# Kernel optimization log

Measured on AMD Instinct MI355X. Metric: run time of the kernel, lower is better.

## Reference

```python
import jax, jax.numpy as jnp
import numpy as np

B, H, S, D1, D2 = 1, 8, 4096, 64, 64


def setup_inputs() -> dict:
    key = jax.random.key(0)
    ks = jax.random.split(key, 6)
    q = jax.random.normal(ks[0], (B, H, S, D1), dtype=jnp.float32)
    k = jax.random.normal(ks[1], (B, H, S, D1), dtype=jnp.float32)
    v = jax.random.normal(ks[2], (B, H, S, D2), dtype=jnp.float32)
    # Decay coefficients per head/position (positive, like RetNet gamma^i masks)
    coef_q = jax.random.uniform(ks[3], (H, S), dtype=jnp.float32)
    coef_k = jax.random.uniform(ks[4], (H, S), dtype=jnp.float32)
    # Normalizer must be bounded away from 0
    mask_normer = jax.random.uniform(ks[5], (H, S), dtype=jnp.float32) + 0.5
    return {"q": q, "k": k, "v": v, "coef_q": coef_q, "coef_k": coef_k,
            "mask_normer": mask_normer}


def _rmsenorm(x):
    return x * jax.lax.rsqrt(jnp.mean(x * x, axis=-1, keepdims=True) + 1e-6)


def reference(q, k, v, coef_q, coef_k, mask_normer):
    # q,k: [B,H,S,D1]; v: [B,H,S,D2]; coef_*/mask_normer: [H,S]
    q_bar = q * (coef_q / mask_normer)[None, :, :, None]      # [B,H,S,D1]
    k_bar = k * coef_k[None, :, :, None]                       # [B,H,S,D1]
    # running normalization P_i = |q_i . sum_{j<=i} k_j|, clamped at 1
    T = jnp.cumsum(k_bar, axis=-2)                             # [B,H,S,D1]
    P = jnp.einsum('bhid,bhid->bhi', T, q_bar)                 # [B,H,S]
    P = jnp.maximum(jnp.abs(jax.lax.stop_gradient(P)), 1.0)[..., None]
    q_bar = q_bar / P
    # outer-product state and prefix sum over sequence
    D = jnp.einsum('bhia,bhic->bhiac', k_bar, v)               # [B,H,S,D1,D2]
    D = jnp.cumsum(D, axis=-3)                                 # cumsum over S
    O = jnp.einsum('bhia,bhiac->bhic', q_bar, D)               # [B,H,S,D2]
    return _rmsenorm(O)
```

## Files before the change

### kernel.cpp

```cpp
#include <hip/hip_runtime.h>

#define H 8
#define S 4096
#define D 64
#define C 64
#define NC (S / C)
#define PITCH 72

typedef short bf16x8 __attribute__((ext_vector_type(8)));
typedef float f32x4 __attribute__((ext_vector_type(4)));

struct alignas(16) F4 { float v[4]; };

__device__ inline short rne_bf16(float x) {
  unsigned u = __builtin_bit_cast(unsigned, x);
  unsigned r = u + 0x7fffu + ((u >> 16) & 1u);
  return (short)(r >> 16);
}
__device__ inline float bf16_to_f(short h) {
  unsigned u = ((unsigned)(unsigned short)h) << 16;
  return __builtin_bit_cast(float, u);
}

__global__ __launch_bounds__(256) void k_chunk_sums(
    const float* __restrict__ k, const float* __restrict__ v,
    const float* __restrict__ coef_k, float* __restrict__ wsKV) {
  const int ch = blockIdx.x, h = blockIdx.y, t = threadIdx.x;
  __shared__ float kb[C][D + 4];
  __shared__ float vb[C][D + 4];

  const float* kp = k + (size_t)(h * S + ch * C) * D;
  const float* vp = v + (size_t)(h * S + ch * C) * D;
  const float* ck = coef_k + h * S + ch * C;

#pragma unroll
  for (int r = 0; r < 4; ++r) {
    int o = 1024 * r + 4 * t;
    int i = o >> 6, d = o & 63;
    F4 kv = *reinterpret_cast<const F4*>(kp + o);
    F4 vv = *reinterpret_cast<const F4*>(vp + o);
    float c = ck[i];
#pragma unroll
    for (int u = 0; u < 4; ++u) kv.v[u] *= c;
    *reinterpret_cast<F4*>(&kb[i][d]) = kv;
    *reinterpret_cast<F4*>(&vb[i][d]) = vv;
  }
  __syncthreads();

  const int tc = t >> 4, ta = t & 15;
  float acc[4][4];
#pragma unroll
  for (int a = 0; a < 4; ++a)
#pragma unroll
    for (int b = 0; b < 4; ++b) acc[a][b] = 0.f;

  for (int i = 0; i < C; ++i) {
    F4 vc = *reinterpret_cast<const F4*>(&vb[i][4 * tc]);
    F4 ka = *reinterpret_cast<const F4*>(&kb[i][4 * ta]);
#pragma unroll
    for (int cc = 0; cc < 4; ++cc)
#pragma unroll
      for (int aa = 0; aa < 4; ++aa) acc[cc][aa] += vc.v[cc] * ka.v[aa];
  }
  float* dst = wsKV + (size_t)(h * NC + ch) * (D * D);
#pragma unroll
  for (int cc = 0; cc < 4; ++cc) {
    F4 w;
#pragma unroll
    for (int aa = 0; aa < 4; ++aa) w.v[aa] = acc[cc][aa];
    *reinterpret_cast<F4*>(dst + (4 * tc + cc) * D + 4 * ta) = w;
  }
}

__global__ __launch_bounds__(128) void k_scan(float* __restrict__ wsKV) {
  const int seg = blockIdx.x, h = blockIdx.y, t = threadIdx.x;
  const int e0 = seg * 128 + t;
  unsigned* wp = reinterpret_cast<unsigned*>(wsKV);
  float run = 0.f;
  for (int base = 0; base < NC; base += 8) {
    float x[8];
#pragma unroll
    for (int u = 0; u < 8; ++u)
      x[u] = wsKV[(size_t)(h * NC + base + u) * (D * D) + e0];
#pragma unroll
    for (int u = 0; u < 8; ++u) {
      short hi = rne_bf16(run);
      short lo = rne_bf16(run - bf16_to_f(hi));
      wp[(size_t)(h * NC + base + u) * (D * D) + e0] =
          (((unsigned)(unsigned short)lo) << 16) | (unsigned)(unsigned short)hi;
      run += x[u];
    }
  }
}

__global__ __launch_bounds__(256) void k_chunk_out(
    const float* __restrict__ q, const float* __restrict__ k,
    const float* __restrict__ v,
    const float* __restrict__ coef_q, const float* __restrict__ coef_k,
    const float* __restrict__ mask_normer,
    const float* __restrict__ wsKV, float* __restrict__ out) {
  const int ch = blockIdx.x, h = blockIdx.y, t = threadIdx.x;
  __shared__ alignas(16) short qb[C * PITCH];
  __shared__ alignas(16) short kbf[C * PITCH];
  __shared__ alignas(16) short s0h[D * PITCH];
  __shared__ alignas(16) short s0l[D * PITCH];
  __shared__ alignas(16) short vT[D * PITCH];
  __shared__ alignas(16) short Ab[C * PITCH];

  const size_t base = (size_t)(h * S + ch * C) * D;
  const float* qp = q + base;
  const float* kp = k + base;
  const float* cq = coef_q + h * S + ch * C;
  const float* ck = coef_k + h * S + ch * C;
  const float* mn = mask_normer + h * S + ch * C;
  const unsigned* s0p =
      reinterpret_cast<const unsigned*>(wsKV) + (size_t)(h * NC + ch) * (D * D);

  {
    const int i = t >> 2, c0 = (t & 3) * 16;
    const float sq = cq[i] / mn[i];
    const float sk = ck[i];
    bf16x8 wq[2], wk[2], wh[2], wl[2];
#pragma unroll
    for (int g = 0; g < 2; ++g) {
#pragma unroll
      for (int u0 = 0; u0 < 8; u0 += 4) {
        F4 qv = *reinterpret_cast<const F4*>(qp + i * D + c0 + 8 * g + u0);
        F4 kv = *reinterpret_cast<const F4*>(kp + i * D + c0 + 8 * g + u0);
#pragma unroll
        for (int u = 0; u < 4; ++u) {
          wq[g][u0 + u] = rne_bf16(qv.v[u] * sq);
          wk[g][u0 + u] = rne_bf16(kv.v[u] * sk);
        }
      }
#pragma unroll
      for (int u = 0; u < 8; ++u) {
        unsigned p = s0p[i * D + c0 + 8 * g + u];
        wh[g][u] = (short)(p & 0xffffu);
        wl[g][u] = (short)(p >> 16);
      }
    }
#pragma unroll
    for (int g = 0; g < 2; ++g) {
      *reinterpret_cast<bf16x8*>(&qb[i * PITCH + c0 + 8 * g]) = wq[g];
      *reinterpret_cast<bf16x8*>(&kbf[i * PITCH + c0 + 8 * g]) = wk[g];
      *reinterpret_cast<bf16x8*>(&s0h[i * PITCH + c0 + 8 * g]) = wh[g];
      *reinterpret_cast<bf16x8*>(&s0l[i * PITCH + c0 + 8 * g]) = wl[g];
    }
  }
  {
    const int c = t >> 2, i0 = (t & 3) * 16;
    const float* vcol = v + base + c;
    bf16x8 wv[2];
#pragma unroll
    for (int g = 0; g < 2; ++g)
#pragma unroll
      for (int u = 0; u < 8; ++u)
        wv[g][u] = rne_bf16(vcol[(size_t)(i0 + 8 * g + u) * D]);
    *reinterpret_cast<bf16x8*>(&vT[c * PITCH + i0]) = wv[0];
    *reinterpret_cast<bf16x8*>(&vT[c * PITCH + i0 + 8]) = wv[1];
  }
  __syncthreads();

  const int lane = t & 63, w = t >> 6;
  const int arow = lane & 15, kg = lane >> 4;
  const int rbase = (16 * w + arow) * PITCH + 8 * kg;

  bf16x8 qa0 = *reinterpret_cast<const bf16x8*>(&qb[rbase]);
  bf16x8 qa1 = *reinterpret_cast<const bf16x8*>(&qb[rbase + 32]);

  f32x4 accA[4];
#pragma unroll
  for (int n = 0; n < 4; ++n) {
    const int bb = (16 * n + arow) * PITCH + 8 * kg;
    bf16x8 b0 = *reinterpret_cast<const bf16x8*>(&kbf[bb]);
    bf16x8 b1 = *reinterpret_cast<const bf16x8*>(&kbf[bb + 32]);
    f32x4 z = {0.f, 0.f, 0.f, 0.f};
    z = __builtin_amdgcn_mfma_f32_16x16x32_bf16(qa0, b0, z, 0, 0, 0);
    z = __builtin_amdgcn_mfma_f32_16x16x32_bf16(qa1, b1, z, 0, 0, 0);
    accA[n] = z;
  }
#pragma unroll
  for (int n = 0; n < 4; ++n)
#pragma unroll
    for (int r = 0; r < 4; ++r) {
      int i = 4 * kg + r;
      int j = 16 * n + arow;
      float x = (j <= 16 * w + i) ? accA[n][r] : 0.f;
      Ab[(16 * w + i) * PITCH + j] = rne_bf16(x);
    }

  bf16x8 aa0 = *reinterpret_cast<const bf16x8*>(&Ab[rbase]);
  bf16x8 aa1 = *reinterpret_cast<const bf16x8*>(&Ab[rbase + 32]);
  f32x4 accO[4];
#pragma unroll
  for (int n = 0; n < 4; ++n) {
    const int bb = (16 * n + arow) * PITCH + 8 * kg;
    bf16x8 h0 = *reinterpret_cast<const bf16x8*>(&s0h[bb]);
    bf16x8 h1 = *reinterpret_cast<const bf16x8*>(&s0h[bb + 32]);
    bf16x8 l0 = *reinterpret_cast<const bf16x8*>(&s0l[bb]);
    bf16x8 l1 = *reinterpret_cast<const bf16x8*>(&s0l[bb + 32]);
    bf16x8 v0 = *reinterpret_cast<const bf16x8*>(&vT[bb]);
    bf16x8 v1 = *reinterpret_cast<const bf16x8*>(&vT[bb + 32]);
    f32x4 z = {0.f, 0.f, 0.f, 0.f};
    z = __builtin_amdgcn_mfma_f32_16x16x32_bf16(qa0, h0, z, 0, 0, 0);
    z = __builtin_amdgcn_mfma_f32_16x16x32_bf16(qa1, h1, z, 0, 0, 0);
    z = __builtin_amdgcn_mfma_f32_16x16x32_bf16(qa0, l0, z, 0, 0, 0);
    z = __builtin_amdgcn_mfma_f32_16x16x32_bf16(qa1, l1, z, 0, 0, 0);
    z = __builtin_amdgcn_mfma_f32_16x16x32_bf16(aa0, v0, z, 0, 0, 0);
    z = __builtin_amdgcn_mfma_f32_16x16x32_bf16(aa1, v1, z, 0, 0, 0);
    accO[n] = z;
  }

  float* op = out + base;
#pragma unroll
  for (int r = 0; r < 4; ++r) {
    const int i = 16 * w + 4 * kg + r;
    float ss = 0.f;
#pragma unroll
    for (int n = 0; n < 4; ++n) ss += accO[n][r] * accO[n][r];
#pragma unroll
    for (int off = 1; off < 16; off <<= 1) ss += __shfl_xor(ss, off);
    const float sc = rsqrtf(ss * (1.0f / D) + 1e-6f);
#pragma unroll
    for (int n = 0; n < 4; ++n)
      op[(size_t)i * D + 16 * n + arow] = accO[n][r] * sc;
  }
}

extern "C" void kernel_launch(void* const* d_in, const int* in_sizes, int n_in,
                              void* d_out, int out_size, void* d_ws, size_t ws_size,
                              hipStream_t stream) {
  (void)in_sizes; (void)n_in; (void)out_size; (void)ws_size;
  const float* q  = (const float*)d_in[0];
  const float* k  = (const float*)d_in[1];
  const float* v  = (const float*)d_in[2];
  const float* cq = (const float*)d_in[3];
  const float* ck = (const float*)d_in[4];
  const float* mn = (const float*)d_in[5];
  float* out = (float*)d_out;

  float* wsKV = (float*)d_ws;

  k_chunk_sums<<<dim3(NC, H), dim3(256), 0, stream>>>(k, v, ck, wsKV);
  k_scan<<<dim3(32, H), dim3(128), 0, stream>>>(wsKV);
  k_chunk_out<<<dim3(NC, H), dim3(256), 0, stream>>>(q, k, v, cq, ck, mn, wsKV, out);
}
```

Before: 27.89 us.

## Use bf16 MFMA for chunk sums and stage v transpose through shared memory

Replaces the scalar FP32 outer-product accumulation in k_chunk_sums with bf16 MFMA, after transposing scaled k and v into bf16 shared tiles. In k_chunk_out, v is now loaded coalesced into shared FP32 and then transposed, instead of strided global loads, and the state loads are vectorized. The scan unroll grows from 8 to 16. Rounding k·v chunk sums to bf16 costs accuracy, and the extra barriers and shared memory may lower occupancy.

```diff
diff --git a/kernel.cpp b/kernel.cpp
--- a/kernel.cpp
+++ b/kernel.cpp
@@ -6,9 +6,11 @@
 #define C 64
 #define NC (S / C)
 #define PITCH 72
+#define FP 68
 
 typedef short bf16x8 __attribute__((ext_vector_type(8)));
 typedef float f32x4 __attribute__((ext_vector_type(4)));
+typedef unsigned uint4v __attribute__((ext_vector_type(4)));
 
 struct alignas(16) F4 { float v[4]; };
 
@@ -26,8 +28,10 @@
     const float* __restrict__ k, const float* __restrict__ v,
     const float* __restrict__ coef_k, float* __restrict__ wsKV) {
   const int ch = blockIdx.x, h = blockIdx.y, t = threadIdx.x;
-  __shared__ float kb[C][D + 4];
-  __shared__ float vb[C][D + 4];
+  __shared__ float kb[C * FP];
+  __shared__ float vb[C * FP];
+  __shared__ alignas(16) short kT[D * PITCH];
+  __shared__ alignas(16) short vT[D * PITCH];
 
   const float* kp = k + (size_t)(h * S + ch * C) * D;
   const float* vp = v + (size_t)(h * S + ch * C) * D;
@@ -42,33 +46,45 @@
     float c = ck[i];
 #pragma unroll
     for (int u = 0; u < 4; ++u) kv.v[u] *= c;
-    *reinterpret_cast<F4*>(&kb[i][d]) = kv;
-    *reinterpret_cast<F4*>(&vb[i][d]) = vv;
-  }
-  __syncthreads();
-
-  const int tc = t >> 4, ta = t & 15;
-  float acc[4][4];
-#pragma unroll
-  for (int a = 0; a < 4; ++a)
-#pragma unroll
-    for (int b = 0; b < 4; ++b) acc[a][b] = 0.f;
-
-  for (int i = 0; i < C; ++i) {
-    F4 vc = *reinterpret_cast<const F4*>(&vb[i][4 * tc]);
-    F4 ka = *reinterpret_cast<const F4*>(&kb[i][4 * ta]);
-#pragma unroll
-    for (int cc = 0; cc < 4; ++cc)
-#pragma unroll
-      for (int aa = 0; aa < 4; ++aa) acc[cc][aa] += vc.v[cc] * ka.v[aa];
-  }
+    *reinterpret_cast<F4*>(&kb[i * FP + d]) = kv;
+    *reinterpret_cast<F4*>(&vb[i * FP + d]) = vv;
+  }
+  __syncthreads();
+
+  {
+    const int col = t & 63, i0 = 16 * (t >> 6);
+    bf16x8 wk[2], wv[2];
+#pragma unroll
+    for (int g = 0; g < 2; ++g)
+#pragma unroll
+      for (int u = 0; u < 8; ++u) {
+        wk[g][u] = rne_bf16(kb[(i0 + 8 * g + u) * FP + col]);
+        wv[g][u] = rne_bf16(vb[(i0 + 8 * g + u) * FP + col]);
+      }
+    *reinterpret_cast<bf16x8*>(&kT[col * PITCH + i0]) = wk[0];
+    *reinterpret_cast<bf16x8*>(&kT[col * PITCH + i0 + 8]) = wk[1];
+    *reinterpret_cast<bf16x8*>(&vT[col * PITCH + i0]) = wv[0];
+    *reinterpret_cast<bf16x8*>(&vT[col * PITCH + i0 + 8]) = wv[1];
+  }
+  __syncthreads();
+
+  const int lane = t & 63, w = t >> 6;
+  const int arow = lane & 15, kg = lane >> 4;
+  const int abase = (16 * w + arow) * PITCH + 8 * kg;
+  bf16x8 a0 = *reinterpret_cast<const bf16x8*>(&vT[abase]);
+  bf16x8 a1 = *reinterpret_cast<const bf16x8*>(&vT[abase + 32]);
   float* dst = wsKV + (size_t)(h * NC + ch) * (D * D);
 #pragma unroll
-  for (int cc = 0; cc < 4; ++cc) {
-    F4 w;
-#pragma unroll
-    for (int aa = 0; aa < 4; ++aa) w.v[aa] = acc[cc][aa];
-    *reinterpret_cast<F4*>(dst + (4 * tc + cc) * D + 4 * ta) = w;
+  for (int n = 0; n < 4; ++n) {
+    const int bb = (16 * n + arow) * PITCH + 8 * kg;
+    bf16x8 b0 = *reinterpret_cast<const bf16x8*>(&kT[bb]);
+    bf16x8 b1 = *reinterpret_cast<const bf16x8*>(&kT[bb + 32]);
+    f32x4 z = {0.f, 0.f, 0.f, 0.f};
+    z = __builtin_amdgcn_mfma_f32_16x16x32_bf16(a0, b0, z, 0, 0, 0);
+    z = __builtin_amdgcn_mfma_f32_16x16x32_bf16(a1, b1, z, 0, 0, 0);
+#pragma unroll
+    for (int r = 0; r < 4; ++r)
+      dst[(16 * w + 4 * kg + r) * D + 16 * n + arow] = z[r];
   }
 }
 
@@ -77,13 +93,13 @@
   const int e0 = seg * 128 + t;
   unsigned* wp = reinterpret_cast<unsigned*>(wsKV);
   float run = 0.f;
-  for (int base = 0; base < NC; base += 8) {
-    float x[8];
-#pragma unroll
-    for (int u = 0; u < 8; ++u)
+  for (int base = 0; base < NC; base += 16) {
+    float x[16];
+#pragma unroll
+    for (int u = 0; u < 16; ++u)
       x[u] = wsKV[(size_t)(h * NC + base + u) * (D * D) + e0];
 #pragma unroll
-    for (int u = 0; u < 8; ++u) {
+    for (int u = 0; u < 16; ++u) {
       short hi = rne_bf16(run);
       short lo = rne_bf16(run - bf16_to_f(hi));
       wp[(size_t)(h * NC + base + u) * (D * D) + e0] =
@@ -106,10 +122,12 @@
   __shared__ alignas(16) short s0l[D * PITCH];
   __shared__ alignas(16) short vT[D * PITCH];
   __shared__ alignas(16) short Ab[C * PITCH];
+  __shared__ float vb[C * FP];
 
   const size_t base = (size_t)(h * S + ch * C) * D;
   const float* qp = q + base;
   const float* kp = k + base;
+  const float* vp = v + base;
   const float* cq = coef_q + h * S + ch * C;
   const float* ck = coef_k + h * S + ch * C;
   const float* mn = mask_normer + h * S + ch * C;
@@ -133,12 +151,19 @@
           wk[g][u0 + u] = rne_bf16(kv.v[u] * sk);
         }
       }
-#pragma unroll
-      for (int u = 0; u < 8; ++u) {
-        unsigned p = s0p[i * D + c0 + 8 * g + u];
-        wh[g][u] = (short)(p & 0xffffu);
-        wl[g][u] = (short)(p >> 16);
-      }
+      uint4v p = *reinterpret_cast<const uint4v*>(s0p + i * D + c0 + 8 * g);
+      uint4v p2 = *reinterpret_cast<const uint4v*>(s0p + i * D + c0 + 8 * g + 4);
+#pragma unroll
+      for (int u = 0; u < 4; ++u) {
+        wh[g][u] = (short)(p[u] & 0xffffu);
+        wl[g][u] = (short)(p[u] >> 16);
+        wh[g][u + 4] = (short)(p2[u] & 0xffffu);
+        wl[g][u + 4] = (short)(p2[u] >> 16);
+      }
+      F4 v0 = *reinterpret_cast<const F4*>(vp + i * D + c0 + 8 * g);
+      F4 v1 = *reinterpret_cast<const F4*>(vp + i * D + c0 + 8 * g + 4);
+      *reinterpret_cast<F4*>(&vb[i * FP + c0 + 8 * g]) = v0;
+      *reinterpret_cast<F4*>(&vb[i * FP + c0 + 8 * g + 4]) = v1;
     }
 #pragma unroll
     for (int g = 0; g < 2; ++g) {
@@ -148,19 +173,19 @@
       *reinterpret_cast<bf16x8*>(&s0l[i * PITCH + c0 + 8 * g]) = wl[g];
     }
   }
-  {
-    const int c = t >> 2, i0 = (t & 3) * 16;
-    const float* vcol = v + base + c;
+  __syncthreads();
+
+  {
+    const int col = t & 63, j0 = 16 * (t >> 6);
     bf16x8 wv[2];
 #pragma unroll
     for (int g = 0; g < 2; ++g)
 #pragma unroll
       for (int u = 0; u < 8; ++u)
-        wv[g][u] = rne_bf16(vcol[(size_t)(i0 + 8 * g + u) * D]);
-    *reinterpret_cast<bf16x8*>(&vT[c * PITCH + i0]) = wv[0];
-    *reinterpret_cast<bf16x8*>(&vT[c * PITCH + i0 + 8]) = wv[1];
-  }
-  __syncthreads();
+        wv[g][u] = rne_bf16(vb[(j0 + 8 * g + u) * FP + col]);
+    *reinterpret_cast<bf16x8*>(&vT[col * PITCH + j0]) = wv[0];
+    *reinterpret_cast<bf16x8*>(&vT[col * PITCH + j0 + 8]) = wv[1];
+  }
 
   const int lane = t & 63, w = t >> 6;
   const int arow = lane & 15, kg = lane >> 4;
@@ -169,26 +194,29 @@
   bf16x8 qa0 = *reinterpret_cast<const bf16x8*>(&qb[rbase]);
   bf16x8 qa1 = *reinterpret_cast<const bf16x8*>(&qb[rbase + 32]);
 
-  f32x4 accA[4];
-#pragma unroll
-  for (int n = 0; n < 4; ++n) {
-    const int bb = (16 * n + arow) * PITCH + 8 * kg;
-    bf16x8 b0 = *reinterpret_cast<const bf16x8*>(&kbf[bb]);
-    bf16x8 b1 = *reinterpret_cast<const bf16x8*>(&kbf[bb + 32]);
-    f32x4 z = {0.f, 0.f, 0.f, 0.f};
-    z = __builtin_amdgcn_mfma_f32_16x16x32_bf16(qa0, b0, z, 0, 0, 0);
-    z = __builtin_amdgcn_mfma_f32_16x16x32_bf16(qa1, b1, z, 0, 0, 0);
-    accA[n] = z;
-  }
-#pragma unroll
-  for (int n = 0; n < 4; ++n)
-#pragma unroll
-    for (int r = 0; r < 4; ++r) {
-      int i = 4 * kg + r;
-      int j = 16 * n + arow;
-      float x = (j <= 16 * w + i) ? accA[n][r] : 0.f;
-      Ab[(16 * w + i) * PITCH + j] = rne_bf16(x);
-    }
+  {
+    f32x4 accA[4];
+#pragma unroll
+    for (int n = 0; n < 4; ++n) {
+      const int bb = (16 * n + arow) * PITCH + 8 * kg;
+      bf16x8 b0 = *reinterpret_cast<const bf16x8*>(&kbf[bb]);
+      bf16x8 b1 = *reinterpret_cast<const bf16x8*>(&kbf[bb + 32]);
+      f32x4 z = {0.f, 0.f, 0.f, 0.f};
+      z = __builtin_amdgcn_mfma_f32_16x16x32_bf16(qa0, b0, z, 0, 0, 0);
+      z = __builtin_amdgcn_mfma_f32_16x16x32_bf16(qa1, b1, z, 0, 0, 0);
+      accA[n] = z;
+    }
+#pragma unroll
+    for (int n = 0; n < 4; ++n)
+#pragma unroll
+      for (int r = 0; r < 4; ++r) {
+        int i = 4 * kg + r;
+        int j = 16 * n + arow;
+        float x = (j <= 16 * w + i) ? accA[n][r] : 0.f;
+        Ab[(16 * w + i) * PITCH + j] = rne_bf16(x);
+      }
+  }
+  __syncthreads();
 
   bf16x8 aa0 = *reinterpret_cast<const bf16x8*>(&Ab[rbase]);
   bf16x8 aa1 = *reinterpret_cast<const bf16x8*>(&Ab[rbase + 32]);
```

New measurement: 25.62 us. 8.1% less time.
